# Kernel optimization log

Measured on AMD Instinct MI355X. Metric: run time of the kernel, lower is better.

Reference implementation:

```python
import jax, jax.numpy as jnp
import numpy as np

# LIFNeuronFDE constants (from init_kwargs)
TAU = 0.5          # membrane time constant (tau_learnable=False)
THRESH = 1.0       # firing threshold V_th
SCALE = 5.0        # surrogate steepness
BETA = 0.5         # fractional order
H = 1.0            # step size h
T, B, N = 32, 32, 32768


def setup_inputs() -> dict:
    key = jax.random.key(0)
    k1, k2 = jax.random.split(key)
    I = jax.random.normal(k1, (T, B, N), dtype=jnp.float32)
    v0 = 0.1 * jax.random.normal(k2, (B, N), dtype=jnp.float32)
    return {"I": I, "v0": v0}


def _gl_coeffs(T_steps: int, beta: float) -> jnp.ndarray:
    # c_0 = 1, c_j = (1 - (1+beta)/j) * c_{j-1}  -> length T+1
    j = np.arange(1, T_steps + 1, dtype=np.float64)
    c = np.concatenate([[1.0], np.cumprod(1.0 - (1.0 + beta) / j)])
    return jnp.asarray(c, dtype=jnp.float32)


def reference(I, v0):
    # Fractional-order LIF with Grunwald-Letnikov memory:
    #   v^{k+1} = h^beta * (-v^k + I^k)/tau - sum_{j=0}^{k} c_{k+1-j} v^{(j)}
    #   spike   = sigmoid(scale * (v - V_th))   (continuous surrogate spike)
    Tn = I.shape[0]
    c = _gl_coeffs(Tn, BETA)                       # (T+1,)
    h_beta = jnp.float32(H ** BETA)
    jidx = jnp.arange(Tn)                          # history slot indices

    def step(carry, I_k):
        v, hist, k = carry                         # hist: (T, B, N)
        hist = hist.at[k].set(v)                   # store v^{(k)} in history buffer
        # coefficient c_{k+1-j} applied to v^{(j)} for j <= k; 0 for unwritten slots
        w = jnp.where(jidx <= k, jnp.take(c, jnp.clip(k + 1 - jidx, 0, Tn)), 0.0)
        mem_sum = jnp.einsum('t,tbn->bn', w, hist)  # GL memory term
        v_next = h_beta * (-v + I_k) / TAU - mem_sum
        spike = jax.nn.sigmoid(SCALE * (v_next - THRESH))
        return (v_next, hist, k + 1), spike

    hist0 = jnp.zeros((Tn,) + v0.shape, v0.dtype)
    _, spikes = jax.lax.scan(step, (v0, hist0, jnp.int32(0)), I)
    return spikes  # (T, B, N) continuous spike outputs
```

## Files before the change

kernel.cpp:

```cpp
#include <hip/hip_runtime.h>
#include <math.h>


#define T_STEPS 32
#define BN (32 * 32768)

struct Coef { double c[T_STEPS + 1]; };

constexpr Coef make_coef() {
    Coef r{};
    r.c[0] = 1.0;
    double cur = 1.0;
    for (int j = 1; j <= T_STEPS; ++j) {
        cur *= (1.0 - 1.5 / (double)j);
        r.c[j] = cur;
    }
    return r;
}

__global__ __launch_bounds__(256) void lif_fde_kernel(
    const float* __restrict__ I,
    const float* __restrict__ v0,
    float* __restrict__ out)
{
    constexpr Coef C = make_coef();

    const int idx = blockIdx.x * blockDim.x + threadIdx.x;

    double v = (double)v0[idx];

    double h[T_STEPS];

    #pragma unroll
    for (int k = 0; k < T_STEPS; ++k) {
        h[k] = v;

        double m = 0.0;
        #pragma unroll
        for (int j = 0; j <= k; ++j) {
            m = fma(C.c[k + 1 - j], h[j], m);
        }

        const float Ik = I[(size_t)k * BN + idx];

        v = 2.0 * ((double)Ik - v) - m;

        const float a = (float)(-5.0 * (v - 1.0));
        out[(size_t)k * BN + idx] = 1.0f / (1.0f + __expf(a));
    }
}

extern "C" void kernel_launch(void* const* d_in, const int* in_sizes, int n_in,
                              void* d_out, int out_size, void* d_ws, size_t ws_size,
                              hipStream_t stream) {
    const float* I  = (const float*)d_in[0];
    const float* v0 = (const float*)d_in[1];
    float* out = (float*)d_out;

    dim3 block(256);
    dim3 grid(BN / 256);
    lif_fde_kernel<<<grid, block, 0, stream>>>(I, v0, out);
}
```

Measured before the change: 60.70 us.

## Precompute closed-form linear map from inputs to membrane voltages

The fractional recurrence is linear, so the constant coefficients mapping v0 and each input I_j to every v_k are computed at compile time. Each output becomes a dot product over the inputs that does not depend on earlier voltages. That removes the serial dependency chain and exposes instruction-level parallelism. It also loads all 32 inputs up front and raises launch bounds to request two blocks per CU; holding 32 doubles per thread risks register pressure.

```diff
diff --git a/kernel.cpp b/kernel.cpp
--- a/kernel.cpp
+++ b/kernel.cpp
@@ -5,47 +5,58 @@
 #define T_STEPS 32
 #define BN (32 * 32768)
 
-struct Coef { double c[T_STEPS + 1]; };
+struct LinMap {
+    double a[T_STEPS][T_STEPS];
+    double b[T_STEPS];
+};
 
-constexpr Coef make_coef() {
-    Coef r{};
-    r.c[0] = 1.0;
-    double cur = 1.0;
-    for (int j = 1; j <= T_STEPS; ++j) {
-        cur *= (1.0 - 1.5 / (double)j);
-        r.c[j] = cur;
+constexpr LinMap make_linmap() {
+    double c[T_STEPS + 1] = {};
+    c[0] = 1.0;
+    for (int j = 1; j <= T_STEPS; ++j) c[j] = c[j - 1] * (1.0 - 1.5 / (double)j);
+
+    double vc[T_STEPS + 1][T_STEPS + 1] = {};
+    vc[0][0] = 1.0;
+
+    LinMap r{};
+    for (int k = 0; k < T_STEPS; ++k) {
+        for (int m = 0; m <= T_STEPS; ++m) {
+            double acc = -2.0 * vc[k][m];
+            for (int j = 0; j <= k; ++j) acc -= c[k + 1 - j] * vc[j][m];
+            vc[k + 1][m] = acc;
+        }
+        vc[k + 1][1 + k] += 2.0;
+
+        r.b[k] = vc[k + 1][0];
+        for (int j = 0; j < T_STEPS; ++j) r.a[k][j] = vc[k + 1][1 + j];
     }
     return r;
 }
 
-__global__ __launch_bounds__(256) void lif_fde_kernel(
+constexpr LinMap CM = make_linmap();
+
+__global__ __launch_bounds__(256, 2) void lif_fde_kernel(
     const float* __restrict__ I,
     const float* __restrict__ v0,
     float* __restrict__ out)
 {
-    constexpr Coef C = make_coef();
-
     const int idx = blockIdx.x * blockDim.x + threadIdx.x;
 
-    double v = (double)v0[idx];
-
-    double h[T_STEPS];
+    double Id[T_STEPS];
+    #pragma unroll
+    for (int k = 0; k < T_STEPS; ++k) {
+        Id[k] = (double)I[(size_t)k * BN + idx];
+    }
+    const double v0d = (double)v0[idx];
 
     #pragma unroll
     for (int k = 0; k < T_STEPS; ++k) {
-        h[k] = v;
-
-        double m = 0.0;
+        double s = CM.b[k] * v0d;
         #pragma unroll
         for (int j = 0; j <= k; ++j) {
-            m = fma(C.c[k + 1 - j], h[j], m);
+            s = fma(CM.a[k][j], Id[j], s);
         }
-
-        const float Ik = I[(size_t)k * BN + idx];
-
-        v = 2.0 * ((double)Ik - v) - m;
-
-        const float a = (float)(-5.0 * (v - 1.0));
+        const float a = (float)(-5.0 * (s - 1.0));
         out[(size_t)k * BN + idx] = 1.0f / (1.0f + __expf(a));
     }
 }
```

Result: no change. 61.23 us (+0.9%).
